# Kernel tuning notes

Hardware: AMD Instinct MI355X
Metric: run time of the kernel (lower is better)

The kernel has to match this reference:

```python
import jax, jax.numpy as jnp
import numpy as np
import math
from fractions import Fraction

# ---- sizes ----
N = 20000        # nodes
C = 64           # channels per body order
LZ = 10          # chemical species (node_attr width)
D = 9            # irreps_sh = 1x0e+1x1o+1x2e -> dim 9
SLICES = {0: (0, 1), 1: (1, 4), 2: (4, 9)}
# parity-allowed (l1,l2,l3) paths for (0e+1o+2e) x (0e+1o+2e) -> (0e+1o+2e)
PATHS = [(0,0,0),(0,1,1),(0,2,2),(1,0,1),(1,1,0),(1,1,2),(1,2,1),(2,0,2),(2,1,1),(2,2,0),(2,2,2)]

# ---- real Wigner 3j in the e3nn convention, computed once in numpy ----
def _cg_coeff(j1, m1, j2, m2, j3, m3):
    if m3 != m1 + m2:
        return 0.0
    f = math.factorial
    vmin = max(-j1 + j2 + m3, -j1 + m1, 0)
    vmax = min(j2 + j3 + m1, j3 - j1 + j2, j3 + m3)
    c = math.sqrt((2 * j3 + 1) * Fraction(
        f(j3 + j1 - j2) * f(j3 - j1 + j2) * f(j1 + j2 - j3) * f(j3 + m3) * f(j3 - m3),
        f(j1 + j2 + j3 + 1) * f(j1 - m1) * f(j1 + m1) * f(j2 - m2) * f(j2 + m2)))
    s = Fraction(0)
    for v in range(vmin, vmax + 1):
        s += (-1) ** (v + j2 + m2) * Fraction(
            f(j2 + j3 + m1 - v) * f(j1 - m1 + v),
            f(v) * f(j3 - j1 + j2 - v) * f(j3 + m3 - v) * f(v + j1 - j2 - m3))
    return c * float(s)

def _su2_cg(j1, j2, j3):
    mat = np.zeros((2 * j1 + 1, 2 * j2 + 1, 2 * j3 + 1))
    for m1 in range(-j1, j1 + 1):
        for m2 in range(-j2, j2 + 1):
            m3 = m1 + m2
            if abs(m3) <= j3:
                mat[j1 + m1, j2 + m2, j3 + m3] = _cg_coeff(j1, m1, j2, m2, j3, m3)
    return mat / math.sqrt(2 * j3 + 1)

def _q(l):
    # real -> complex spherical-harmonic change of basis (e3nn convention)
    q = np.zeros((2 * l + 1, 2 * l + 1), dtype=complex)
    for m in range(-l, 0):
        q[l + m, l + abs(m)] = 1 / math.sqrt(2)
        q[l + m, l - abs(m)] = -1j / math.sqrt(2)
    q[l, l] = 1.0
    for m in range(1, l + 1):
        q[l + m, l + abs(m)] = (-1) ** m / math.sqrt(2)
        q[l + m, l - abs(m)] = 1j * (-1) ** m / math.sqrt(2)
    return (-1j) ** l * q

def _wigner_3j(l1, l2, l3):
    Cc = _su2_cg(l1, l2, l3).astype(complex)
    Cc = np.einsum('ij,kl,mn,ikn->jlm', _q(l1), _q(l2), np.conj(_q(l3).T), Cc)
    assert np.abs(Cc.imag).max() < 1e-6
    return np.real(Cc).astype(np.float32)

W3J = {p: jnp.asarray(_wigner_3j(*p)) for p in PATHS}

def _contract(t1, t2):
    # t1, t2: (N, M, D) with irreps 1x0e+1x1o+1x2e on the last axis
    acc = {0: None, 1: None, 2: None}
    for (l1, l2, l3) in PATHS:
        a1, b1 = SLICES[l1]
        a2, b2 = SLICES[l2]
        c = jnp.einsum('ncl,ncm,lms->ncs', t1[..., a1:b1], t2[..., a2:b2], W3J[(l1, l2, l3)])
        acc[l3] = c if acc[l3] is None else acc[l3] + c
    return jnp.concatenate([acc[0], acc[1], acc[2]], axis=-1)

def _forward(node_nbody, node_attr, W_chem, W_body):
    n0, n1, n2 = node_nbody[0], node_nbody[1], node_nbody[2]
    nodes, channels, d = n0.shape
    lenz = node_attr.shape[1]
    # pack 3 body orders: (N,C,D,3) -> (N,D,C,3) -> (N,D,3C) -> (N,3C,D)
    node3 = jnp.stack((n0, n1, n2), axis=-1)
    node3 = jnp.transpose(node3, (0, 2, 1, 3)).reshape(nodes, d, 3 * channels)
    node3 = jnp.transpose(node3, (0, 2, 1))
    # (3,N,L) -> (3,L,N) -> (N,3L)  (faithful to the torch reshape, incl. its element ordering)
    nab = jnp.stack((node_attr, node_attr, node_attr), axis=0)
    nab = jnp.transpose(nab, (0, 2, 1)).reshape(nodes, 3 * lenz)
    # e3nn Linear on scalars: x @ W / sqrt(fan_in)
    wz = (nab @ W_chem) / np.float32(math.sqrt(3 * lenz))                 # (N, D*3C)
    wz = jnp.transpose(wz.reshape(nodes, d, 3 * channels), (0, 2, 1))     # (N, 3C, D)
    m = _contract(wz, node3)                                              # (N, 3C, D)
    m = jnp.transpose(m, (0, 2, 1)).reshape(nodes * channels * d, 3)
    out = (m @ W_body) / np.float32(math.sqrt(3.0))                       # Linear 3x0e -> 1x0e
    return jnp.transpose(out.reshape(nodes, d, channels), (0, 2, 1))      # (N, C, D)

def setup_inputs() -> dict:
    key = jax.random.key(0)
    k1, k2, k3, k4 = jax.random.split(key, 4)
    return {
        'node_nbody': jax.random.normal(k1, (3, N, C, D), dtype=jnp.float32),
        'node_attr': jax.random.normal(k2, (N, LZ), dtype=jnp.float32),
        'W_chem': jax.random.normal(k3, (3 * LZ, D * 3 * C), dtype=jnp.float32),
        'W_body': jax.random.normal(k4, (3, 1), dtype=jnp.float32),
    }

def reference(node_nbody, node_attr, W_chem, W_body):
    return _forward(node_nbody, node_attr, W_chem, W_body)
```

## Files before the change

### kernel.cpp

```cpp
#include <hip/hip_runtime.h>

#define N_NODES 20000
#define WCB_FLOATS (3*9*30*64)
#define NAB_FLOATS (N_NODES*32)

struct kx { double re, im; };

__host__ __device__ constexpr kx kmul(kx a, kx b){
  return { a.re*b.re - a.im*b.im, a.re*b.im + a.im*b.re };
}

__host__ __device__ constexpr double cfact(int n){
  double r = 1.0; for (int i = 2; i <= n; ++i) r *= (double)i; return r;
}

__host__ __device__ constexpr double csqrt(double x){
  if (x <= 0.0) return 0.0;
  double g = x > 1.0 ? x : 1.0;
  for (int i = 0; i < 64; ++i) g = 0.5*(g + x/g);
  return g;
}

__host__ __device__ constexpr double ccg(int j1,int m1,int j2,int m2,int j3,int m3){
  if (m3 != m1 + m2) return 0.0;
  int vmin = -j1 + j2 + m3;
  if (-j1 + m1 > vmin) vmin = -j1 + m1;
  if (vmin < 0) vmin = 0;
  int vmax = j2 + j3 + m1;
  if (j3 - j1 + j2 < vmax) vmax = j3 - j1 + j2;
  if (j3 + m3 < vmax) vmax = j3 + m3;
  double c = csqrt((double)(2*j3+1) *
      (cfact(j3+j1-j2)*cfact(j3-j1+j2)*cfact(j1+j2-j3)*cfact(j3+m3)*cfact(j3-m3)) /
      (cfact(j1+j2+j3+1)*cfact(j1-m1)*cfact(j1+m1)*cfact(j2-m2)*cfact(j2+m2)));
  double s = 0.0;
  for (int v = vmin; v <= vmax; ++v){
    double t = (cfact(j2+j3+m1-v)*cfact(j1-m1+v)) /
               (cfact(v)*cfact(j3-j1+j2-v)*cfact(j3+m3-v)*cfact(v+j1-j2-m3));
    s += ((v + j2 + m2) & 1) ? -t : t;
  }
  return c * s;
}

__host__ __device__ constexpr kx cq(int l, int r, int c){
  kx v = {0.0, 0.0};
  const double is2 = 0.70710678118654752440;
  const int m = r - l;
  if (m < 0){
    if (c == 2*l - r)      v = { is2, 0.0 };
    else if (c == r)       v = { 0.0, -is2 };
  } else if (m == 0){
    if (c == l)            v = { 1.0, 0.0 };
  } else {
    const double sg = (m & 1) ? -1.0 : 1.0;
    if (c == r)            v = { sg*is2, 0.0 };
    else if (c == 2*l - r) v = { 0.0, sg*is2 };
  }
  if (l == 1)      v = { v.im, -v.re };
  else if (l == 2) v = { -v.re, -v.im };
  return v;
}

__host__ __device__ constexpr double cw_entry(int L, int M, int S){
  const int l1 = (L==0)?0:((L<4)?1:2);
  const int l2 = (M==0)?0:((M<4)?1:2);
  const int l3 = (S==0)?0:((S<4)?1:2);
  const int a  = L - ((l1==0)?0:((l1==1)?1:4));
  const int b  = M - ((l2==0)?0:((l2==1)?1:4));
  const int cc = S - ((l3==0)?0:((l3==1)?1:4));
  const int lo = (l1 > l2) ? l1 - l2 : l2 - l1;
  if (!(l3 >= lo && l3 <= l1 + l2 && (((l1 + l2 + l3) & 1) == 0))) return 0.0;
  double ar = 0.0, ai = 0.0;
  for (int i = 0; i < 2*l1+1; ++i){
    kx q1 = cq(l1, i, a);
    if (q1.re == 0.0 && q1.im == 0.0) continue;
    for (int k = 0; k < 2*l2+1; ++k){
      kx q2 = cq(l2, k, b);
      if (q2.re == 0.0 && q2.im == 0.0) continue;
      kx q12 = kmul(q1, q2);
      for (int n = 0; n < 2*l3+1; ++n){
        kx q3 = cq(l3, n, cc);
        if (q3.re == 0.0 && q3.im == 0.0) continue;
        double cg = ccg(l1, i-l1, l2, k-l2, l3, n-l3);
        if (cg == 0.0) continue;
        kx q3c = { q3.re, -q3.im };
        kx term = kmul(q12, q3c);
        ar += term.re * cg;
        ai += term.im * cg;
      }
    }
  }
  const double w = ar / csqrt((double)(2*l3+1));
  return w * 0.10540925533894598;
}

__global__ void nn3b_init_kernel(const float* __restrict__ node_attr,
                                 const float* __restrict__ W_chem,
                                 const float* __restrict__ wbody,
                                 float* __restrict__ wcB,
                                 float* __restrict__ nab)
{
  const int t = blockIdx.x * 256 + threadIdx.x;

  if (t < WCB_FLOATS){
    const int c = t & 63;
    const int k = (t >> 6) % 30;
    const int d = (t / 1920) % 9;
    const int b = t / 17280;
    wcB[t] = W_chem[k*1728 + d*192 + 3*c + b] * wbody[b];
  }

  const int tc = t - WCB_FLOATS;
  if (tc >= 0 && tc < NAB_FLOATS){
    const int n = tc >> 5;
    const int k = tc & 31;
    float v = 0.0f;
    if (k < 30){
      const int i = 30*n + k;
      v = node_attr[(i % N_NODES)*10 + ((i / N_NODES) % 10)];
    }
    nab[tc] = v;
  }
}


#define STAGE(Q)                                                          \
  __syncthreads();                                                        \
  {                                                                       \
    const float4* src4 = (const float4*)(wcb_b + (Q)*5760);               \
    float4* dst4 = (float4*)ldsw;                                         \
    dst4[tid]       = src4[tid];                                          \
    dst4[tid + 512] = src4[tid + 512];                                    \
    if (tid < 416) dst4[tid + 1024] = src4[tid + 1024];                   \
  }                                                                       \
  __syncthreads();

#define UCOMP(SLAB)                                                       \
  {                                                                       \
    float a0=0.f, a1=0.f, b0=0.f, b1=0.f;                                 \
    const float* wp = ldsw + (SLAB)*1920 + c;                             \
    _Pragma("unroll")                                                     \
    for (int k = 0; k < 15; ++k){                                         \
      const float w0 = wp[k*64];                                          \
      const float w1 = wp[(k+15)*64];                                     \
      a0 = fmaf(nabA[k],    w0, a0);                                      \
      a1 = fmaf(nabA[k+15], w1, a1);                                      \
      b0 = fmaf(nabB[k],    w0, b0);                                      \
      b1 = fmaf(nabB[k+15], w1, b1);                                      \
    }                                                                     \
    uA = a0 + a1; uB = b0 + b1;                                           \
  }

#define E(DL,M,S)                                                         \
  {                                                                       \
    constexpr float cc_ = (float)cw_entry(DL,M,S);                        \
    oA[S] = fmaf(cc_ * uA, vA[M], oA[S]);                                 \
    oB[S] = fmaf(cc_ * uB, vB[M], oB[S]);                                 \
  }

#define LD9(dst, p) { dst[0]=(p)[0]; dst[1]=(p)[1]; dst[2]=(p)[2];        \
                      dst[3]=(p)[3]; dst[4]=(p)[4]; dst[5]=(p)[5];        \
                      dst[6]=(p)[6]; dst[7]=(p)[7]; dst[8]=(p)[8]; }
#define ST9(p, src) { (p)[0]=src[0]; (p)[1]=src[1]; (p)[2]=src[2];        \
                      (p)[3]=src[3]; (p)[4]=src[4]; (p)[5]=src[5];        \
                      (p)[6]=src[6]; (p)[7]=src[7]; (p)[8]=src[8]; }

__global__ __launch_bounds__(512)
void nn3b_main_kernel(const float* __restrict__ nbody,
                      const float* __restrict__ wcB,
                      const float* __restrict__ nab,
                      float* __restrict__ out)
{
  __shared__ __align__(16) float ldsw[5760];

  const int tid = threadIdx.x;
  const int c   = tid & 63;
  const int g   = __builtin_amdgcn_readfirstlane((int)(tid >> 6));
  const int nA  = blockIdx.x * 16 + g * 2;
  const int nB  = nA + 1;

  float oA[9] = {0,0,0,0,0,0,0,0,0};
  float oB[9] = {0,0,0,0,0,0,0,0,0};

  const float* nabA = nab + (size_t)nA * 32;
  const float* nabB = nab + (size_t)nB * 32;

  #pragma unroll 1
  for (int b = 0; b < 3; ++b){
    float vA[9], vB[9];
    {
      const float* pA = nbody + ((size_t)b*N_NODES + nA)*576 + c*9;
      const float* pB = nbody + ((size_t)b*N_NODES + nB)*576 + c*9;
      LD9(vA, pA);
      LD9(vB, pB);
    }
    const float* wcb_b = wcB + b*(9*30*64);
    float uA, uB;

    STAGE(0)
    UCOMP(0)
    E(0,0,0) E(0,1,1) E(0,2,2) E(0,3,3) E(0,4,4) E(0,5,5) E(0,6,6) E(0,7,7) E(0,8,8)
    UCOMP(1)
    E(1,0,1) E(1,1,0) E(1,3,4) E(1,2,5) E(1,1,6) E(1,1,8) E(1,4,3) E(1,5,2) E(1,6,1) E(1,8,1)
    UCOMP(2)
    E(2,0,2) E(2,2,0) E(2,1,5) E(2,3,7) E(2,2,6) E(2,5,1) E(2,7,3) E(2,6,2)

    STAGE(1)
    UCOMP(0)
    E(3,0,3) E(3,3,0) E(3,1,4) E(3,2,7) E(3,3,6) E(3,3,8) E(3,4,1) E(3,7,2) E(3,6,3) E(3,8,3)
    UCOMP(1)
    E(4,0,4) E(4,4,0) E(4,1,3) E(4,3,1) E(4,6,4) E(4,4,6) E(4,5,7) E(4,7,5)
    UCOMP(2)
    E(5,0,5) E(5,5,0) E(5,1,2) E(5,2,1) E(5,6,5) E(5,5,6) E(5,5,8) E(5,8,5) E(5,4,7) E(5,7,4)

    STAGE(2)
    UCOMP(0)
    E(6,0,6) E(6,6,0) E(6,1,1) E(6,2,2) E(6,3,3) E(6,6,6) E(6,5,5) E(6,7,7) E(6,4,4) E(6,8,8)
    UCOMP(1)
    E(7,0,7) E(7,7,0) E(7,2,3) E(7,3,2) E(7,6,7) E(7,7,6) E(7,7,8) E(7,8,7) E(7,4,5) E(7,5,4)
    UCOMP(2)
    E(8,0,8) E(8,8,0) E(8,1,1) E(8,3,3) E(8,6,8) E(8,8,6) E(8,5,5) E(8,7,7)
  }

  {
    float* pA = out + (size_t)nA*576 + c*9;
    float* pB = out + (size_t)nB*576 + c*9;
    ST9(pA, oA);
    ST9(pB, oB);
  }
}

extern "C" void kernel_launch(void* const* d_in, const int* in_sizes, int n_in,
                              void* d_out, int out_size, void* d_ws, size_t ws_size,
                              hipStream_t stream)
{
  const float* nbody     = (const float*)d_in[0];
  const float* node_attr = (const float*)d_in[1];
  const float* W_chem    = (const float*)d_in[2];
  const float* wbody     = (const float*)d_in[3];
  float* out = (float*)d_out;

  float* wcB = (float*)d_ws;
  float* nab = wcB + WCB_FLOATS;

  const int init_items  = WCB_FLOATS + NAB_FLOATS;
  const int init_blocks = (init_items + 255) / 256;
  nn3b_init_kernel<<<init_blocks, 256, 0, stream>>>(node_attr, W_chem, wbody, wcB, nab);

  nn3b_main_kernel<<<N_NODES/16, 512, 0, stream>>>(nbody, wcB, nab, out);
}
```

Measured before the change: 298.0 us.

## Split fused kernel into chemistry-weight kernel and contraction kernel via workspace

Replaces the single fused kernel with two kernels when the workspace is large enough. The first computes the per-node chemistry weights u with weights held in registers and writes them to a 3*N*9*64 float buffer. The second reads u and node_nbody and does the Clebsch-Gordan contraction with no LDS staging or barriers. The aim is to remove the repeated LDS weight staging and syncs, at the cost of writing and re-reading about 138 MB of intermediate through HBM.

```diff
diff --git a/kernel.cpp b/kernel.cpp
--- a/kernel.cpp
+++ b/kernel.cpp
@@ -3,6 +3,7 @@
 #define N_NODES 20000
 #define WCB_FLOATS (3*9*30*64)
 #define NAB_FLOATS (N_NODES*32)
+#define U_FLOATS   (3*N_NODES*9*64)
 
 struct kx { double re, im; };
 
@@ -122,6 +123,102 @@
   }
 }
 
+__global__ __launch_bounds__(256)
+void nn3b_u_kernel(const float* __restrict__ wcB,
+                   const float* __restrict__ nab,
+                   float* __restrict__ u_out)
+{
+  const int tid = threadIdx.x;
+  const int c   = tid & 63;
+  const int W   = __builtin_amdgcn_readfirstlane(blockIdx.x * 4 + (tid >> 6));
+  const int g   = W % 9;
+  const int b   = g / 3;
+  const int s3  = g % 3;
+  const int n0  = (W / 9) * 25;
+
+  float w0[30], w1[30], w2[30];
+  {
+    const float* base = wcB + (size_t)((b*9 + s3*3)*30)*64 + c;
+    #pragma unroll
+    for (int k = 0; k < 30; ++k){
+      w0[k] = base[(size_t)k*64];
+      w1[k] = base[(size_t)(30 + k)*64];
+      w2[k] = base[(size_t)(60 + k)*64];
+    }
+  }
+
+  float* uo = u_out + ((size_t)(b*N_NODES + n0)*9 + s3*3)*64 + c;
+  const float* na = nab + (size_t)n0*32;
+
+  for (int i = 0; i < 25; ++i){
+    float a0=0.f, a1=0.f, b0=0.f, b1=0.f, c0=0.f, c1=0.f;
+    #pragma unroll
+    for (int k = 0; k < 15; ++k){
+      const float s0 = na[k];
+      const float s1 = na[k + 15];
+      a0 = fmaf(s0, w0[k],      a0);
+      a1 = fmaf(s1, w0[k + 15], a1);
+      b0 = fmaf(s0, w1[k],      b0);
+      b1 = fmaf(s1, w1[k + 15], b1);
+      c0 = fmaf(s0, w2[k],      c0);
+      c1 = fmaf(s1, w2[k + 15], c1);
+    }
+    uo[0]   = a0 + a1;
+    uo[64]  = b0 + b1;
+    uo[128] = c0 + c1;
+    uo += 9*64;
+    na += 32;
+  }
+}
+
+#define LD9(dst, p) { dst[0]=(p)[0]; dst[1]=(p)[1]; dst[2]=(p)[2];        \
+                      dst[3]=(p)[3]; dst[4]=(p)[4]; dst[5]=(p)[5];        \
+                      dst[6]=(p)[6]; dst[7]=(p)[7]; dst[8]=(p)[8]; }
+#define ST9(p, src) { (p)[0]=src[0]; (p)[1]=src[1]; (p)[2]=src[2];        \
+                      (p)[3]=src[3]; (p)[4]=src[4]; (p)[5]=src[5];        \
+                      (p)[6]=src[6]; (p)[7]=src[7]; (p)[8]=src[8]; }
+
+#define EC(DL,M,S)                                                        \
+  {                                                                       \
+    constexpr float cc_ = (float)cw_entry(DL,M,S);                        \
+    o[S] = fmaf(cc_ * uu[DL], v[M], o[S]);                                \
+  }
+
+__global__ __launch_bounds__(256)
+void nn3b_e_kernel(const float* __restrict__ nbody,
+                   const float* __restrict__ u_in,
+                   float* __restrict__ out)
+{
+  const int t = blockIdx.x * 256 + threadIdx.x;
+  const int c = t & 63;
+  const int n = t >> 6;
+
+  float o[9] = {0,0,0,0,0,0,0,0,0};
+
+  #pragma unroll 1
+  for (int b = 0; b < 3; ++b){
+    float v[9];
+    LD9(v, nbody + (size_t)(b*N_NODES + n)*576 + c*9);
+
+    const float* pu = u_in + (size_t)(b*N_NODES + n)*576 + c;
+    float uu[9];
+    uu[0]=pu[0];   uu[1]=pu[64];  uu[2]=pu[128];
+    uu[3]=pu[192]; uu[4]=pu[256]; uu[5]=pu[320];
+    uu[6]=pu[384]; uu[7]=pu[448]; uu[8]=pu[512];
+
+    EC(0,0,0) EC(0,1,1) EC(0,2,2) EC(0,3,3) EC(0,4,4) EC(0,5,5) EC(0,6,6) EC(0,7,7) EC(0,8,8)
+    EC(1,0,1) EC(1,1,0) EC(1,3,4) EC(1,2,5) EC(1,1,6) EC(1,1,8) EC(1,4,3) EC(1,5,2) EC(1,6,1) EC(1,8,1)
+    EC(2,0,2) EC(2,2,0) EC(2,1,5) EC(2,3,7) EC(2,2,6) EC(2,5,1) EC(2,7,3) EC(2,6,2)
+    EC(3,0,3) EC(3,3,0) EC(3,1,4) EC(3,2,7) EC(3,3,6) EC(3,3,8) EC(3,4,1) EC(3,7,2) EC(3,6,3) EC(3,8,3)
+    EC(4,0,4) EC(4,4,0) EC(4,1,3) EC(4,3,1) EC(4,6,4) EC(4,4,6) EC(4,5,7) EC(4,7,5)
+    EC(5,0,5) EC(5,5,0) EC(5,1,2) EC(5,2,1) EC(5,6,5) EC(5,5,6) EC(5,5,8) EC(5,8,5) EC(5,4,7) EC(5,7,4)
+    EC(6,0,6) EC(6,6,0) EC(6,1,1) EC(6,2,2) EC(6,3,3) EC(6,6,6) EC(6,5,5) EC(6,7,7) EC(6,4,4) EC(6,8,8)
+    EC(7,0,7) EC(7,7,0) EC(7,2,3) EC(7,3,2) EC(7,6,7) EC(7,7,6) EC(7,7,8) EC(7,8,7) EC(7,4,5) EC(7,5,4)
+    EC(8,0,8) EC(8,8,0) EC(8,1,1) EC(8,3,3) EC(8,6,8) EC(8,8,6) EC(8,5,5) EC(8,7,7)
+  }
+
+  ST9(out + (size_t)t*9, o);
+}
 
 #define STAGE(Q)                                                          \
   __syncthreads();                                                        \
@@ -157,13 +254,6 @@
     oB[S] = fmaf(cc_ * uB, vB[M], oB[S]);                                 \
   }
 
-#define LD9(dst, p) { dst[0]=(p)[0]; dst[1]=(p)[1]; dst[2]=(p)[2];        \
-                      dst[3]=(p)[3]; dst[4]=(p)[4]; dst[5]=(p)[5];        \
-                      dst[6]=(p)[6]; dst[7]=(p)[7]; dst[8]=(p)[8]; }
-#define ST9(p, src) { (p)[0]=src[0]; (p)[1]=src[1]; (p)[2]=src[2];        \
-                      (p)[3]=src[3]; (p)[4]=src[4]; (p)[5]=src[5];        \
-                      (p)[6]=src[6]; (p)[7]=src[7]; (p)[8]=src[8]; }
-
 __global__ __launch_bounds__(512)
 void nn3b_main_kernel(const float* __restrict__ nbody,
                       const float* __restrict__ wcB,
@@ -241,10 +331,17 @@
 
   float* wcB = (float*)d_ws;
   float* nab = wcB + WCB_FLOATS;
+  float* u   = nab + NAB_FLOATS;
 
   const int init_items  = WCB_FLOATS + NAB_FLOATS;
   const int init_blocks = (init_items + 255) / 256;
   nn3b_init_kernel<<<init_blocks, 256, 0, stream>>>(node_attr, W_chem, wbody, wcB, nab);
 
-  nn3b_main_kernel<<<N_NODES/16, 512, 0, stream>>>(nbody, wcB, nab, out);
-}
+  const size_t need = ((size_t)WCB_FLOATS + NAB_FLOATS + U_FLOATS) * sizeof(float);
+  if (ws_size >= need){
+    nn3b_u_kernel<<<1800, 256, 0, stream>>>(wcB, nab, u);
+    nn3b_e_kernel<<<5000, 256, 0, stream>>>(nbody, u, out);
+  } else {
+    nn3b_main_kernel<<<N_NODES/16, 512, 0, stream>>>(nbody, wcB, nab, out);
+  }
+}
```

After: 269.3 us. -9.6%, faster.

## Keep chemical weights in registers and share per-node u via LDS

Applied to the files above, without the earlier changes.

The main kernel is restructured so that each of 9 wavefronts holds a fixed 3-slab slice of the combined chemical weights (90 floats) in registers for the whole block. This replaces re-staging the weights through LDS for every 16-node block. Each wave computes its u values for 9 nodes per group, writes them to LDS, and after a barrier each wave does the Clebsch-Gordan contraction for one node. The grid becomes 445 persistent-ish blocks of 576 threads looping over 5 groups of 9 nodes. This trades heavy weight traffic for high register pressure, lower occupancy and two barriers per group.

```diff
diff --git a/kernel.cpp b/kernel.cpp
--- a/kernel.cpp
+++ b/kernel.cpp
@@ -122,41 +122,6 @@
   }
 }
 
-
-#define STAGE(Q)                                                          \
-  __syncthreads();                                                        \
-  {                                                                       \
-    const float4* src4 = (const float4*)(wcb_b + (Q)*5760);               \
-    float4* dst4 = (float4*)ldsw;                                         \
-    dst4[tid]       = src4[tid];                                          \
-    dst4[tid + 512] = src4[tid + 512];                                    \
-    if (tid < 416) dst4[tid + 1024] = src4[tid + 1024];                   \
-  }                                                                       \
-  __syncthreads();
-
-#define UCOMP(SLAB)                                                       \
-  {                                                                       \
-    float a0=0.f, a1=0.f, b0=0.f, b1=0.f;                                 \
-    const float* wp = ldsw + (SLAB)*1920 + c;                             \
-    _Pragma("unroll")                                                     \
-    for (int k = 0; k < 15; ++k){                                         \
-      const float w0 = wp[k*64];                                          \
-      const float w1 = wp[(k+15)*64];                                     \
-      a0 = fmaf(nabA[k],    w0, a0);                                      \
-      a1 = fmaf(nabA[k+15], w1, a1);                                      \
-      b0 = fmaf(nabB[k],    w0, b0);                                      \
-      b1 = fmaf(nabB[k+15], w1, b1);                                      \
-    }                                                                     \
-    uA = a0 + a1; uB = b0 + b1;                                           \
-  }
-
-#define E(DL,M,S)                                                         \
-  {                                                                       \
-    constexpr float cc_ = (float)cw_entry(DL,M,S);                        \
-    oA[S] = fmaf(cc_ * uA, vA[M], oA[S]);                                 \
-    oB[S] = fmaf(cc_ * uB, vB[M], oB[S]);                                 \
-  }
-
 #define LD9(dst, p) { dst[0]=(p)[0]; dst[1]=(p)[1]; dst[2]=(p)[2];        \
                       dst[3]=(p)[3]; dst[4]=(p)[4]; dst[5]=(p)[5];        \
                       dst[6]=(p)[6]; dst[7]=(p)[7]; dst[8]=(p)[8]; }
@@ -164,68 +129,105 @@
                       (p)[3]=src[3]; (p)[4]=src[4]; (p)[5]=src[5];        \
                       (p)[6]=src[6]; (p)[7]=src[7]; (p)[8]=src[8]; }
 
-__global__ __launch_bounds__(512)
-void nn3b_main_kernel(const float* __restrict__ nbody,
-                      const float* __restrict__ wcB,
-                      const float* __restrict__ nab,
-                      float* __restrict__ out)
+#define EC(DL,M,S)                                                        \
+  {                                                                       \
+    constexpr float cc_ = (float)cw_entry(DL,M,S);                        \
+    o[S] = fmaf(cc_ * uu[DL], v[M], o[S]);                                \
+  }
+
+#define EC_TABLE                                                          \
+  EC(0,0,0) EC(0,1,1) EC(0,2,2) EC(0,3,3) EC(0,4,4) EC(0,5,5) EC(0,6,6) EC(0,7,7) EC(0,8,8) \
+  EC(1,0,1) EC(1,1,0) EC(1,3,4) EC(1,2,5) EC(1,1,6) EC(1,1,8) EC(1,4,3) EC(1,5,2) EC(1,6,1) EC(1,8,1) \
+  EC(2,0,2) EC(2,2,0) EC(2,1,5) EC(2,3,7) EC(2,2,6) EC(2,5,1) EC(2,7,3) EC(2,6,2) \
+  EC(3,0,3) EC(3,3,0) EC(3,1,4) EC(3,2,7) EC(3,3,6) EC(3,3,8) EC(3,4,1) EC(3,7,2) EC(3,6,3) EC(3,8,3) \
+  EC(4,0,4) EC(4,4,0) EC(4,1,3) EC(4,3,1) EC(4,6,4) EC(4,4,6) EC(4,5,7) EC(4,7,5) \
+  EC(5,0,5) EC(5,5,0) EC(5,1,2) EC(5,2,1) EC(5,6,5) EC(5,5,6) EC(5,5,8) EC(5,8,5) EC(5,4,7) EC(5,7,4) \
+  EC(6,0,6) EC(6,6,0) EC(6,1,1) EC(6,2,2) EC(6,3,3) EC(6,6,6) EC(6,5,5) EC(6,7,7) EC(6,4,4) EC(6,8,8) \
+  EC(7,0,7) EC(7,7,0) EC(7,2,3) EC(7,3,2) EC(7,6,7) EC(7,7,6) EC(7,7,8) EC(7,8,7) EC(7,4,5) EC(7,5,4) \
+  EC(8,0,8) EC(8,8,0) EC(8,1,1) EC(8,3,3) EC(8,6,8) EC(8,8,6) EC(8,5,5) EC(8,7,7)
+
+#define PHASE2_B(VV, B)                                                   \
+  {                                                                       \
+    float uu[9];                                                          \
+    uu[0]=up[(B)*576+0];   uu[1]=up[(B)*576+64];  uu[2]=up[(B)*576+128];  \
+    uu[3]=up[(B)*576+192]; uu[4]=up[(B)*576+256]; uu[5]=up[(B)*576+320];  \
+    uu[6]=up[(B)*576+384]; uu[7]=up[(B)*576+448]; uu[8]=up[(B)*576+512];  \
+    float v[9];                                                           \
+    v[0]=VV[0]; v[1]=VV[1]; v[2]=VV[2]; v[3]=VV[3]; v[4]=VV[4];           \
+    v[5]=VV[5]; v[6]=VV[6]; v[7]=VV[7]; v[8]=VV[8];                       \
+    EC_TABLE                                                              \
+  }
+
+__global__ __launch_bounds__(576)
+void nn3b_fused_kernel(const float* __restrict__ nbody,
+                       const float* __restrict__ wcB,
+                       const float* __restrict__ nab,
+                       float* __restrict__ out)
 {
-  __shared__ __align__(16) float ldsw[5760];
+  __shared__ __align__(16) float uL[9*27*64];
 
   const int tid = threadIdx.x;
   const int c   = tid & 63;
   const int g   = __builtin_amdgcn_readfirstlane((int)(tid >> 6));
-  const int nA  = blockIdx.x * 16 + g * 2;
-  const int nB  = nA + 1;
-
-  float oA[9] = {0,0,0,0,0,0,0,0,0};
-  float oB[9] = {0,0,0,0,0,0,0,0,0};
-
-  const float* nabA = nab + (size_t)nA * 32;
-  const float* nabB = nab + (size_t)nB * 32;
+  const int b   = g / 3;
+  const int s3  = g - 3*b;
+  const int nbase = blockIdx.x * 45;
+
+  float w0[30], w1[30], w2[30];
+  {
+    const float* base = wcB + (size_t)((b*9 + s3*3)*30)*64 + c;
+    #pragma unroll
+    for (int k = 0; k < 30; ++k){
+      w0[k] = base[(size_t)k*64];
+      w1[k] = base[(size_t)(30+k)*64];
+      w2[k] = base[(size_t)(60+k)*64];
+    }
+  }
 
   #pragma unroll 1
-  for (int b = 0; b < 3; ++b){
-    float vA[9], vB[9];
-    {
-      const float* pA = nbody + ((size_t)b*N_NODES + nA)*576 + c*9;
-      const float* pB = nbody + ((size_t)b*N_NODES + nB)*576 + c*9;
-      LD9(vA, pA);
-      LD9(vB, pB);
-    }
-    const float* wcb_b = wcB + b*(9*30*64);
-    float uA, uB;
-
-    STAGE(0)
-    UCOMP(0)
-    E(0,0,0) E(0,1,1) E(0,2,2) E(0,3,3) E(0,4,4) E(0,5,5) E(0,6,6) E(0,7,7) E(0,8,8)
-    UCOMP(1)
-    E(1,0,1) E(1,1,0) E(1,3,4) E(1,2,5) E(1,1,6) E(1,1,8) E(1,4,3) E(1,5,2) E(1,6,1) E(1,8,1)
-    UCOMP(2)
-    E(2,0,2) E(2,2,0) E(2,1,5) E(2,3,7) E(2,2,6) E(2,5,1) E(2,7,3) E(2,6,2)
-
-    STAGE(1)
-    UCOMP(0)
-    E(3,0,3) E(3,3,0) E(3,1,4) E(3,2,7) E(3,3,6) E(3,3,8) E(3,4,1) E(3,7,2) E(3,6,3) E(3,8,3)
-    UCOMP(1)
-    E(4,0,4) E(4,4,0) E(4,1,3) E(4,3,1) E(4,6,4) E(4,4,6) E(4,5,7) E(4,7,5)
-    UCOMP(2)
-    E(5,0,5) E(5,5,0) E(5,1,2) E(5,2,1) E(5,6,5) E(5,5,6) E(5,5,8) E(5,8,5) E(5,4,7) E(5,7,4)
-
-    STAGE(2)
-    UCOMP(0)
-    E(6,0,6) E(6,6,0) E(6,1,1) E(6,2,2) E(6,3,3) E(6,6,6) E(6,5,5) E(6,7,7) E(6,4,4) E(6,8,8)
-    UCOMP(1)
-    E(7,0,7) E(7,7,0) E(7,2,3) E(7,3,2) E(7,6,7) E(7,7,6) E(7,7,8) E(7,8,7) E(7,4,5) E(7,5,4)
-    UCOMP(2)
-    E(8,0,8) E(8,8,0) E(8,1,1) E(8,3,3) E(8,6,8) E(8,8,6) E(8,5,5) E(8,7,7)
-  }
-
-  {
-    float* pA = out + (size_t)nA*576 + c*9;
-    float* pB = out + (size_t)nB*576 + c*9;
-    ST9(pA, oA);
-    ST9(pB, oB);
+  for (int grp = 0; grp < 5; ++grp){
+    const int n2 = nbase + grp*9 + g;
+
+    float v0[9], v1[9], v2[9];
+    if (n2 < N_NODES){
+      LD9(v0, nbody + ((size_t)(0*N_NODES + n2))*576 + c*9);
+      LD9(v1, nbody + ((size_t)(1*N_NODES + n2))*576 + c*9);
+      LD9(v2, nbody + ((size_t)(2*N_NODES + n2))*576 + c*9);
+    }
+
+    #pragma unroll 1
+    for (int i = 0; i < 9; ++i){
+      const int n = nbase + grp*9 + i;
+      if (n >= N_NODES) break;
+      const float* na = nab + (size_t)n * 32;
+      float a0=0.f, a1=0.f, b0=0.f, b1=0.f, c0=0.f, c1=0.f;
+      #pragma unroll
+      for (int k = 0; k < 15; ++k){
+        const float s0 = na[k];
+        const float s1 = na[k+15];
+        a0 = fmaf(s0, w0[k],    a0);
+        a1 = fmaf(s1, w0[k+15], a1);
+        b0 = fmaf(s0, w1[k],    b0);
+        b1 = fmaf(s1, w1[k+15], b1);
+        c0 = fmaf(s0, w2[k],    c0);
+        c1 = fmaf(s1, w2[k+15], c1);
+      }
+      float* uw = uL + (i*27 + b*9 + s3*3)*64 + c;
+      uw[0]   = a0 + a1;
+      uw[64]  = b0 + b1;
+      uw[128] = c0 + c1;
+    }
+    __syncthreads();
+
+    if (n2 < N_NODES){
+      float o[9] = {0,0,0,0,0,0,0,0,0};
+      const float* up = uL + (g*27)*64 + c;
+      PHASE2_B(v0, 0)
+      PHASE2_B(v1, 1)
+      PHASE2_B(v2, 2)
+      ST9(out + (size_t)n2*576 + c*9, o);
+    }
+    __syncthreads();
   }
 }
 
@@ -246,5 +248,5 @@
   const int init_blocks = (init_items + 255) / 256;
   nn3b_init_kernel<<<init_blocks, 256, 0, stream>>>(node_attr, W_chem, wbody, wcB, nab);
 
-  nn3b_main_kernel<<<N_NODES/16, 512, 0, stream>>>(nbody, wcB, nab, out);
-}
+  nn3b_fused_kernel<<<445, 576, 0, stream>>>(nbody, wcB, nab, out);
+}
```

Measured after the change: 446.6 us. 1.5x slower.
